# Performance work log

Hardware: AMD Instinct MI355X
Metric: run time of the kernel (lower is better)

Reference implementation:

```python
import jax, jax.numpy as jnp
import numpy as np

H = 512

def _lstm_dir(seq, Wih, Whh, bih, bhh, reverse):
    # seq: [B,S,in]; Wih: [4H,in]; Whh: [4H,H]; biases [4H]
    B = seq.shape[0]
    xp = jnp.einsum('bsi,gi->bsg', seq, Wih) + bih  # precompute input projection [B,S,4H]
    h0 = jnp.zeros((B, H), seq.dtype)
    c0 = jnp.zeros((B, H), seq.dtype)

    def step(carry, xt):
        h, c = carry
        g = xt + h @ Whh.T + bhh
        i, f, gg, o = jnp.split(g, 4, axis=-1)
        c = jax.nn.sigmoid(f) * c + jax.nn.sigmoid(i) * jnp.tanh(gg)
        h = jax.nn.sigmoid(o) * jnp.tanh(c)
        return (h, c), h

    _, hs = jax.lax.scan(step, (h0, c0), jnp.swapaxes(xp, 0, 1), reverse=reverse)
    return jnp.swapaxes(hs, 0, 1)  # [B,S,H]


def setup_inputs() -> dict:
    key = jax.random.key(0)
    ks = jax.random.split(key, 24)
    B, S, E, V, C = 32, 512, 512, 32000, 2
    sc = 0.1
    d = {
        'x': jax.random.randint(ks[0], (B, S), 0, V, dtype=jnp.int32),
        'attention_mask': jnp.ones((B, S), dtype=jnp.int32),
        'emb': jax.random.normal(ks[1], (V, E), jnp.float32) * sc,
        'fc_W': jax.random.normal(ks[2], (C, 2 * H), jnp.float32) * sc,
        'fc_b': jax.random.normal(ks[3], (C,), jnp.float32) * sc,
    }
    i = 4
    for l, insz in [(0, E), (1, 2 * H)]:
        for dname in ('fwd', 'bwd'):
            d[f'{dname}_Wih{l}'] = jax.random.normal(ks[i], (4 * H, insz), jnp.float32) * sc; i += 1
            d[f'{dname}_Whh{l}'] = jax.random.normal(ks[i], (4 * H, H), jnp.float32) * sc; i += 1
            d[f'{dname}_bih{l}'] = jax.random.normal(ks[i], (4 * H,), jnp.float32) * sc; i += 1
            d[f'{dname}_bhh{l}'] = jax.random.normal(ks[i], (4 * H,), jnp.float32) * sc; i += 1
    return d


def reference(x, attention_mask, emb, fc_W, fc_b,
              fwd_Wih0, fwd_Whh0, fwd_bih0, fwd_bhh0,
              bwd_Wih0, bwd_Whh0, bwd_bih0, bwd_bhh0,
              fwd_Wih1, fwd_Whh1, fwd_bih1, fwd_bhh1,
              bwd_Wih1, bwd_Whh1, bwd_bih1, bwd_bhh1):
    out = emb[x]  # [B,S,E]
    layers = [
        ((fwd_Wih0, fwd_Whh0, fwd_bih0, fwd_bhh0), (bwd_Wih0, bwd_Whh0, bwd_bih0, bwd_bhh0)),
        ((fwd_Wih1, fwd_Whh1, fwd_bih1, fwd_bhh1), (bwd_Wih1, bwd_Whh1, bwd_bih1, bwd_bhh1)),
    ]
    for fw, bw in layers:
        f = _lstm_dir(out, *fw, reverse=False)
        b = _lstm_dir(out, *bw, reverse=True)
        out = jnp.concatenate([f, b], axis=-1)  # [B,S,2H]
        # dropout is identity in eval mode
    mask = attention_mask.astype(out.dtype)
    pooled = (out * mask[..., None]).sum(axis=1) / jnp.clip(mask.sum(axis=1, keepdims=True), 1e-9)
    logits = pooled @ fc_W.T + fc_b
    return logits
```

## Files before the change

kernel.cpp:

```cpp
#include <hip/hip_runtime.h>

typedef unsigned short u16;
typedef unsigned int   u32;
typedef unsigned long long u64;
typedef __attribute__((ext_vector_type(8))) short bf16x8;
typedef __attribute__((ext_vector_type(4))) float f32x4;

__device__ __forceinline__ u16 f2bf(float f) {
    u32 u; __builtin_memcpy(&u, &f, 4);
    u32 r = (u + 0x7FFFu + ((u >> 16) & 1u)) >> 16;
    return (u16)r;
}
__device__ __forceinline__ float bf2f(u16 h) {
    u32 u = ((u32)h) << 16; float f; __builtin_memcpy(&f, &u, 4); return f;
}
__device__ __forceinline__ float sigmoidf(float x) { return 1.f / (1.f + __expf(-x)); }
__device__ __forceinline__ float tanh_safe(float x) {
    float e = __expf(-2.f * fabsf(x));
    float t = (1.f - e) / (1.f + e);
    return x >= 0.f ? t : -t;
}

__global__ __launch_bounds__(256) void castk2(const float* __restrict__ s, u16* __restrict__ hi,
                                              u16* __restrict__ lo, int n) {
    int i = blockIdx.x * 256 + threadIdx.x;
    if (i < n) {
        float f = s[i];
        u16 h = f2bf(f);
        hi[i] = h;
        lo[i] = f2bf(f - bf2f(h));
    }
}

__global__ __launch_bounds__(256) void embed_cast(const int* __restrict__ x, const float* __restrict__ emb,
                                                  u16* __restrict__ x0) {
    int m = blockIdx.x;
    int idx = x[m];
    const float2* src = (const float2*)(emb + (size_t)idx * 512);
    u16* dst = x0 + (size_t)m * 512;
    int t = threadIdx.x;
    float2 v = src[t];
    dst[t * 2]     = f2bf(v.x);
    dst[t * 2 + 1] = f2bf(v.y);
}

__global__ __launch_bounds__(256) void gemm_bt(const u16* __restrict__ A, const u16* __restrict__ Bhi,
                                               const u16* __restrict__ Blo,
                                               u16* __restrict__ C, int M, int N, int K) {
    __shared__ __align__(16) u16 sA[128 * 32];
    __shared__ __align__(16) u16 sBh[128 * 32];
    __shared__ __align__(16) u16 sBl[128 * 32];
    const int tid  = threadIdx.x;
    const int lane = tid & 63, wave = tid >> 6;
    const int m0 = blockIdx.y * 128, n0 = blockIdx.x * 128;
    const int wm = (wave >> 1) * 64, wn = (wave & 1) * 64;
    f32x4 acc[4][4] = {};

    const int r0 = tid >> 2, c8 = (tid & 3) * 8;
    const int r1 = r0 + 64;
    const u16* Ap   = A   + (size_t)(m0 + r0) * K + c8;
    const u16* Ap2  = A   + (size_t)(m0 + r1) * K + c8;
    const u16* Bhp  = Bhi + (size_t)(n0 + r0) * K + c8;
    const u16* Bhp2 = Bhi + (size_t)(n0 + r1) * K + c8;
    const u16* Blp  = Blo + (size_t)(n0 + r0) * K + c8;
    const u16* Blp2 = Blo + (size_t)(n0 + r1) * K + c8;

    uint4 ra0, ra1, rh0, rh1, rl0, rl1;
    ra0 = *(const uint4*)(Ap);   ra1 = *(const uint4*)(Ap2);
    rh0 = *(const uint4*)(Bhp);  rh1 = *(const uint4*)(Bhp2);
    rl0 = *(const uint4*)(Blp);  rl1 = *(const uint4*)(Blp2);

    for (int kk = 0; kk < K; kk += 32) {
        __syncthreads();
        *(uint4*)(sA  + tid * 8)        = ra0;
        *(uint4*)(sA  + 2048 + tid * 8) = ra1;
        *(uint4*)(sBh + tid * 8)        = rh0;
        *(uint4*)(sBh + 2048 + tid * 8) = rh1;
        *(uint4*)(sBl + tid * 8)        = rl0;
        *(uint4*)(sBl + 2048 + tid * 8) = rl1;
        int kn = kk + 32;
        if (kn < K) {
            ra0 = *(const uint4*)(Ap + kn);   ra1 = *(const uint4*)(Ap2 + kn);
            rh0 = *(const uint4*)(Bhp + kn);  rh1 = *(const uint4*)(Bhp2 + kn);
            rl0 = *(const uint4*)(Blp + kn);  rl1 = *(const uint4*)(Blp2 + kn);
        }
        __syncthreads();
        bf16x8 av[4], bh[4], bl[4];
#pragma unroll
        for (int i = 0; i < 4; ++i) {
            av[i] = *(const bf16x8*)(sA  + (wm + i * 16 + (lane & 15)) * 32 + (lane >> 4) * 8);
            bh[i] = *(const bf16x8*)(sBh + (wn + i * 16 + (lane & 15)) * 32 + (lane >> 4) * 8);
            bl[i] = *(const bf16x8*)(sBl + (wn + i * 16 + (lane & 15)) * 32 + (lane >> 4) * 8);
        }
#pragma unroll
        for (int i = 0; i < 4; ++i)
#pragma unroll
            for (int j = 0; j < 4; ++j) {
                acc[i][j] = __builtin_amdgcn_mfma_f32_16x16x32_bf16(av[i], bh[j], acc[i][j], 0, 0, 0);
                acc[i][j] = __builtin_amdgcn_mfma_f32_16x16x32_bf16(av[i], bl[j], acc[i][j], 0, 0, 0);
            }
    }
#pragma unroll
    for (int i = 0; i < 4; ++i) {
        int m = m0 + wm + i * 16 + ((lane >> 4) << 2);
#pragma unroll
        for (int j = 0; j < 4; ++j) {
            int n = n0 + wn + j * 16 + (lane & 15);
#pragma unroll
            for (int rr = 0; rr < 4; ++rr)
                C[(size_t)(m + rr) * N + n] = f2bf(acc[i][j][rr]);
        }
    }
}

template <int LAYER>
__global__ __launch_bounds__(256, 1) void lstm_rec(
    const u16* __restrict__ xp_f, const u16* __restrict__ xp_b,
    const u16* __restrict__ whh_f_hi, const u16* __restrict__ whh_f_lo,
    const u16* __restrict__ whh_b_hi, const u16* __restrict__ whh_b_lo,
    const float* __restrict__ bih_f, const float* __restrict__ bhh_f,
    const float* __restrict__ bih_b, const float* __restrict__ bhh_b,
    u16* __restrict__ out0, float* __restrict__ pooled, const int* __restrict__ mask,
    u16* hbuf, u32* cnt)
{
    const int HP = 520;
    __shared__ __align__(16) u16  sHhi[32 * 520];
    __shared__ __align__(16) u16  sHlo[32 * 520];
    __shared__ __align__(16) u16  sXp[32 * 32];
    __shared__ __align__(16) float sG[32 * 33];
    __shared__ __align__(16) u16  sHoutHi[32 * 8];
    __shared__ __align__(16) u16  sHoutLo[32 * 8];

    const int tid = threadIdx.x;
    const int dir = blockIdx.x >> 6;
    const int slice = blockIdx.x & 63;
    const u16* xp     = dir ? xp_b : xp_f;
    const u16* whhH   = dir ? whh_b_hi : whh_f_hi;
    const u16* whhL   = dir ? whh_b_lo : whh_f_lo;
    const float* bih  = dir ? bih_b : bih_f;
    const float* bhh  = dir ? bhh_b : bhh_f;
    u16* hbD = hbuf + dir * 65536;
    u32* myFlags = cnt + dir * 64;

    const int wave = tid >> 6, lane = tid & 63;
    const int wm = (wave >> 1) * 16;
    const int wn = (wave & 1) * 16;
    bf16x8 wfragH[16], wfragL[16];
    {
        int n = wn + (lane & 15);
        int q = n >> 3, rr = n & 7;
        size_t rowoff = (size_t)(q * 512 + slice * 8 + rr) * 512 + (lane >> 4) * 8;
        const u16* wrh = whhH + rowoff;
        const u16* wrl = whhL + rowoff;
#pragma unroll
        for (int k2 = 0; k2 < 16; ++k2) {
            wfragH[k2] = *(const bf16x8*)(wrh + k2 * 32);
            wfragL[k2] = *(const bf16x8*)(wrl + k2 * 32);
        }
    }
    const int b = tid >> 3, r = tid & 7;
    float bias[4];
#pragma unroll
    for (int q = 0; q < 4; ++q) {
        int g = q * 512 + slice * 8 + r;
        bias[q] = bih[g] + bhh[g];
    }
    float cstate = 0.f, pool = 0.f;
    const int aoff = (wm + (lane & 15)) * HP + (lane >> 4) * 8;
    const int gRow = wm + ((lane >> 4) << 2), gCol = wn + (lane & 15);
    const int srow = tid >> 3, sc = tid & 7;

    for (int t = 0; t < 512; ++t) {
        const int tt = dir ? (511 - t) : t;
        if (tid < 128) {
            int xb = tid >> 2, xq = tid & 3;
            const uint4 v = *(const uint4*)(xp + ((size_t)(xb * 512 + tt)) * 2048 + xq * 512 + slice * 8);
            *(uint4*)(sXp + xb * 32 + xq * 8) = v;
        }
        if (t > 0 && tid < 64) {
            const u32 tgt = (u32)t;
            for (;;) {
                u32 v = __hip_atomic_load(myFlags + tid, __ATOMIC_RELAXED, __HIP_MEMORY_SCOPE_AGENT);
                if (__all((int)(v >= tgt))) break;
                __builtin_amdgcn_s_sleep(1);
            }
        }
        __syncthreads();
        if (t > 0) {
            const u16* hp = hbD + ((t - 1) & 1) * 32768 + srow * 512;
            const u16* lp = hp + 16384;
            u16* dhi = sHhi + srow * HP;
            u16* dlo = sHlo + srow * HP;
            u64 rh[16], rl[16];
#pragma unroll
            for (int j = 0; j < 8; ++j) {
                int ch = sc + 8 * j;
                rh[2*j]   = __hip_atomic_load((const u64*)(hp + ch * 8),     __ATOMIC_RELAXED, __HIP_MEMORY_SCOPE_AGENT);
                rh[2*j+1] = __hip_atomic_load((const u64*)(hp + ch * 8) + 1, __ATOMIC_RELAXED, __HIP_MEMORY_SCOPE_AGENT);
                rl[2*j]   = __hip_atomic_load((const u64*)(lp + ch * 8),     __ATOMIC_RELAXED, __HIP_MEMORY_SCOPE_AGENT);
                rl[2*j+1] = __hip_atomic_load((const u64*)(lp + ch * 8) + 1, __ATOMIC_RELAXED, __HIP_MEMORY_SCOPE_AGENT);
            }
#pragma unroll
            for (int j = 0; j < 8; ++j) {
                int ch = sc + 8 * j;
                *(u64*)(dhi + ch * 8)     = rh[2*j];
                *(u64*)(dhi + ch * 8 + 4) = rh[2*j+1];
                *(u64*)(dlo + ch * 8)     = rl[2*j];
                *(u64*)(dlo + ch * 8 + 4) = rl[2*j+1];
            }
        }
        __syncthreads();
        f32x4 acc = {};
        if (t > 0) {
#pragma unroll
            for (int k2 = 0; k2 < 16; ++k2) {
                bf16x8 ah = *(const bf16x8*)(sHhi + aoff + k2 * 32);
                bf16x8 al = *(const bf16x8*)(sHlo + aoff + k2 * 32);
                acc = __builtin_amdgcn_mfma_f32_16x16x32_bf16(ah, wfragH[k2], acc, 0, 0, 0);
                acc = __builtin_amdgcn_mfma_f32_16x16x32_bf16(al, wfragH[k2], acc, 0, 0, 0);
                acc = __builtin_amdgcn_mfma_f32_16x16x32_bf16(ah, wfragL[k2], acc, 0, 0, 0);
            }
        }
#pragma unroll
        for (int rr = 0; rr < 4; ++rr) sG[(gRow + rr) * 33 + gCol] = acc[rr];
        __syncthreads();
        {
            float gq[4];
#pragma unroll
            for (int q = 0; q < 4; ++q)
                gq[q] = sG[b * 33 + q * 8 + r] + bf2f(sXp[b * 32 + q * 8 + r]) + bias[q];
            float ig = sigmoidf(gq[0]), fg = sigmoidf(gq[1]);
            float gg = tanh_safe(gq[2]), og = sigmoidf(gq[3]);
            cstate = fg * cstate + ig * gg;
            float h = og * tanh_safe(cstate);
            u16 hh = f2bf(h);
            if (LAYER == 0) {
                out0[((size_t)(b * 512 + tt)) * 1024 + dir * 512 + slice * 8 + r] = hh;
            } else {
                pool += h * (float)mask[b * 512 + tt];
            }
            sHoutHi[b * 8 + r] = hh;
            sHoutLo[b * 8 + r] = f2bf(h - bf2f(hh));
        }
        __syncthreads();
        if (tid < 64) {
#pragma unroll
            for (int j = 0; j < 2; ++j) {
                int w = tid + 64 * j;
                int pb = w >> 2, d = w & 3;
                u32 vh = ((const u32*)sHoutHi)[w];
                u32 vl = ((const u32*)sHoutLo)[w];
                u32* gh = (u32*)(hbD + (t & 1) * 32768 + pb * 512 + slice * 8) + d;
                u32* gl = (u32*)(hbD + (t & 1) * 32768 + 16384 + pb * 512 + slice * 8) + d;
                __hip_atomic_store(gh, vh, __ATOMIC_RELAXED, __HIP_MEMORY_SCOPE_AGENT);
                __hip_atomic_store(gl, vl, __ATOMIC_RELAXED, __HIP_MEMORY_SCOPE_AGENT);
            }
            if (tid == 0)
                __hip_atomic_store(myFlags + slice, (u32)(t + 1), __ATOMIC_RELEASE, __HIP_MEMORY_SCOPE_AGENT);
        }
    }
    if (LAYER == 1)
        pooled[(size_t)b * 1024 + dir * 512 + slice * 8 + r] = pool;
}

__global__ __launch_bounds__(256) void final_fc(const float* __restrict__ pooled, const int* __restrict__ mask,
                                                const float* __restrict__ fcW, const float* __restrict__ fcb,
                                                float* __restrict__ out) {
    __shared__ float red[256];
    int tid = threadIdx.x;
    int pair = tid & 63, kc = tid >> 6;
    int b = pair >> 1, c = pair & 1;
    float s = 0.f;
    for (int k = kc * 256; k < kc * 256 + 256; ++k)
        s += pooled[b * 1024 + k] * fcW[c * 1024 + k];
    red[tid] = s;
    __syncthreads();
    if (kc == 0) {
        float tot = red[pair] + red[64 + pair] + red[128 + pair] + red[192 + pair];
        float ms = 0.f;
        for (int t = 0; t < 512; ++t) ms += (float)mask[b * 512 + t];
        ms = fmaxf(ms, 1e-9f);
        out[b * 2 + c] = tot / ms + fcb[c];
    }
}

extern "C" void kernel_launch(void* const* d_in, const int* in_sizes, int n_in,
                              void* d_out, int out_size, void* d_ws, size_t ws_size,
                              hipStream_t stream) {
    (void)in_sizes; (void)n_in; (void)out_size; (void)ws_size;
    const int*   x     = (const int*)d_in[0];
    const int*   amask = (const int*)d_in[1];
    const float* emb   = (const float*)d_in[2];
    const float* fcW   = (const float*)d_in[3];
    const float* fcb   = (const float*)d_in[4];
    const float* fWih0 = (const float*)d_in[5];
    const float* fWhh0 = (const float*)d_in[6];
    const float* fbih0 = (const float*)d_in[7];
    const float* fbhh0 = (const float*)d_in[8];
    const float* bWih0 = (const float*)d_in[9];
    const float* bWhh0 = (const float*)d_in[10];
    const float* bbih0 = (const float*)d_in[11];
    const float* bbhh0 = (const float*)d_in[12];
    const float* fWih1 = (const float*)d_in[13];
    const float* fWhh1 = (const float*)d_in[14];
    const float* fbih1 = (const float*)d_in[15];
    const float* fbhh1 = (const float*)d_in[16];
    const float* bWih1 = (const float*)d_in[17];
    const float* bWhh1 = (const float*)d_in[18];
    const float* bbih1 = (const float*)d_in[19];
    const float* bbhh1 = (const float*)d_in[20];

    char* ws = (char*)d_ws;
    size_t off = 0;
    auto alloc = [&](size_t bytes) { void* p = ws + off; off += (bytes + 1023) & ~(size_t)1023; return p; };
    u16* x0    = (u16*)alloc((size_t)16384 * 512 * 2);
    u16* xpf   = (u16*)alloc((size_t)16384 * 2048 * 2);
    u16* xpb   = (u16*)alloc((size_t)16384 * 2048 * 2);
    u16* out0  = (u16*)alloc((size_t)16384 * 1024 * 2);
    u16* wih0fH = (u16*)alloc((size_t)2048 * 512 * 2);
    u16* wih0fL = (u16*)alloc((size_t)2048 * 512 * 2);
    u16* wih0bH = (u16*)alloc((size_t)2048 * 512 * 2);
    u16* wih0bL = (u16*)alloc((size_t)2048 * 512 * 2);
    u16* whh0fH = (u16*)alloc((size_t)2048 * 512 * 2);
    u16* whh0fL = (u16*)alloc((size_t)2048 * 512 * 2);
    u16* whh0bH = (u16*)alloc((size_t)2048 * 512 * 2);
    u16* whh0bL = (u16*)alloc((size_t)2048 * 512 * 2);
    u16* wih1fH = (u16*)alloc((size_t)2048 * 1024 * 2);
    u16* wih1fL = (u16*)alloc((size_t)2048 * 1024 * 2);
    u16* wih1bH = (u16*)alloc((size_t)2048 * 1024 * 2);
    u16* wih1bL = (u16*)alloc((size_t)2048 * 1024 * 2);
    u16* whh1fH = (u16*)alloc((size_t)2048 * 512 * 2);
    u16* whh1fL = (u16*)alloc((size_t)2048 * 512 * 2);
    u16* whh1bH = (u16*)alloc((size_t)2048 * 512 * 2);
    u16* whh1bL = (u16*)alloc((size_t)2048 * 512 * 2);
    float* pooled = (float*)alloc((size_t)32 * 1024 * 4);
    u16* hbuf  = (u16*)alloc((size_t)2 * 2 * 2 * 32 * 512 * 2);
    u32* cnt   = (u32*)alloc(1024);

    hipMemsetAsync(cnt, 0, 1024, stream);

    const int NW0 = 2048 * 512, NW1 = 2048 * 1024;
    castk2<<<dim3((NW0 + 255) / 256), 256, 0, stream>>>(fWih0, wih0fH, wih0fL, NW0);
    castk2<<<dim3((NW0 + 255) / 256), 256, 0, stream>>>(bWih0, wih0bH, wih0bL, NW0);
    castk2<<<dim3((NW0 + 255) / 256), 256, 0, stream>>>(fWhh0, whh0fH, whh0fL, NW0);
    castk2<<<dim3((NW0 + 255) / 256), 256, 0, stream>>>(bWhh0, whh0bH, whh0bL, NW0);
    castk2<<<dim3((NW1 + 255) / 256), 256, 0, stream>>>(fWih1, wih1fH, wih1fL, NW1);
    castk2<<<dim3((NW1 + 255) / 256), 256, 0, stream>>>(bWih1, wih1bH, wih1bL, NW1);
    castk2<<<dim3((NW0 + 255) / 256), 256, 0, stream>>>(fWhh1, whh1fH, whh1fL, NW0);
    castk2<<<dim3((NW0 + 255) / 256), 256, 0, stream>>>(bWhh1, whh1bH, whh1bL, NW0);

    embed_cast<<<dim3(16384), 256, 0, stream>>>(x, emb, x0);

    gemm_bt<<<dim3(16, 128), 256, 0, stream>>>(x0, wih0fH, wih0fL, xpf, 16384, 2048, 512);
    gemm_bt<<<dim3(16, 128), 256, 0, stream>>>(x0, wih0bH, wih0bL, xpb, 16384, 2048, 512);
    lstm_rec<0><<<dim3(128), 256, 0, stream>>>(xpf, xpb, whh0fH, whh0fL, whh0bH, whh0bL,
                                               fbih0, fbhh0, bbih0, bbhh0,
                                               out0, nullptr, nullptr, hbuf, cnt);
    gemm_bt<<<dim3(16, 128), 256, 0, stream>>>(out0, wih1fH, wih1fL, xpf, 16384, 2048, 1024);
    gemm_bt<<<dim3(16, 128), 256, 0, stream>>>(out0, wih1bH, wih1bL, xpb, 16384, 2048, 1024);
    lstm_rec<1><<<dim3(128), 256, 0, stream>>>(xpf, xpb, whh1fH, whh1fL, whh1bH, whh1bL,
                                               fbih1, fbhh1, bbih1, bbhh1,
                                               nullptr, pooled, amask, hbuf, cnt + 128);

    final_fc<<<dim3(1), 256, 0, stream>>>(pooled, amask, fcW, fcb, (float*)d_out);
}
```

Baseline: 7.155 ms.

## Publish hidden state per wave with per-wave flags, drop staging barrier

Each thread now writes its own h hi/lo values straight to the global exchange buffer and each wave raises its own ready flag. This removes the shared-memory staging step and one block-wide barrier from the serial critical path of every timestep. Waiters poll four flags per slice using 64-bit loads. The change also splits the MFMA accumulation into three independent chains to shorten the dependency latency, prefetches xp into registers early, and changes the LDS padding. The flag store is now relaxed rather than release, relying on s_waitcnt for ordering, which carries a memory-ordering risk.

```diff
diff --git a/kernel.cpp b/kernel.cpp
--- a/kernel.cpp
+++ b/kernel.cpp
@@ -123,13 +123,10 @@
     u16* __restrict__ out0, float* __restrict__ pooled, const int* __restrict__ mask,
     u16* hbuf, u32* cnt)
 {
-    const int HP = 520;
-    __shared__ __align__(16) u16  sHhi[32 * 520];
-    __shared__ __align__(16) u16  sHlo[32 * 520];
-    __shared__ __align__(16) u16  sXp[32 * 32];
+    const int HP = 524;
+    __shared__ __align__(16) u16  sHhi[32 * 524];
+    __shared__ __align__(16) u16  sHlo[32 * 524];
     __shared__ __align__(16) float sG[32 * 33];
-    __shared__ __align__(16) u16  sHoutHi[32 * 8];
-    __shared__ __align__(16) u16  sHoutLo[32 * 8];
 
     const int tid = threadIdx.x;
     const int dir = blockIdx.x >> 6;
@@ -140,7 +137,7 @@
     const float* bih  = dir ? bih_b : bih_f;
     const float* bhh  = dir ? bhh_b : bhh_f;
     u16* hbD = hbuf + dir * 65536;
-    u32* myFlags = cnt + dir * 64;
+    u32* myFlags = cnt + dir * 256;
 
     const int wave = tid >> 6, lane = tid & 63;
     const int wm = (wave >> 1) * 16;
@@ -169,19 +166,21 @@
     const int aoff = (wm + (lane & 15)) * HP + (lane >> 4) * 8;
     const int gRow = wm + ((lane >> 4) << 2), gCol = wn + (lane & 15);
     const int srow = tid >> 3, sc = tid & 7;
+    const u16* xpBase = xp + (size_t)(b * 512) * 2048 + slice * 8 + r;
 
     for (int t = 0; t < 512; ++t) {
         const int tt = dir ? (511 - t) : t;
-        if (tid < 128) {
-            int xb = tid >> 2, xq = tid & 3;
-            const uint4 v = *(const uint4*)(xp + ((size_t)(xb * 512 + tt)) * 2048 + xq * 512 + slice * 8);
-            *(uint4*)(sXp + xb * 32 + xq * 8) = v;
-        }
+        const u16* xrow = xpBase + (size_t)tt * 2048;
+        u16 xv0 = xrow[0], xv1 = xrow[512], xv2 = xrow[1024], xv3 = xrow[1536];
         if (t > 0 && tid < 64) {
             const u32 tgt = (u32)t;
+            const u64* fp = (const u64*)(myFlags + tid * 4);
             for (;;) {
-                u32 v = __hip_atomic_load(myFlags + tid, __ATOMIC_RELAXED, __HIP_MEMORY_SCOPE_AGENT);
-                if (__all((int)(v >= tgt))) break;
+                u64 f01 = __hip_atomic_load(fp,     __ATOMIC_RELAXED, __HIP_MEMORY_SCOPE_AGENT);
+                u64 f23 = __hip_atomic_load(fp + 1, __ATOMIC_RELAXED, __HIP_MEMORY_SCOPE_AGENT);
+                int ok = ((u32)f01 >= tgt) & ((u32)(f01 >> 32) >= tgt) &
+                         ((u32)f23 >= tgt) & ((u32)(f23 >> 32) >= tgt);
+                if (__all(ok)) break;
                 __builtin_amdgcn_s_sleep(1);
             }
         }
@@ -210,53 +209,44 @@
             }
         }
         __syncthreads();
-        f32x4 acc = {};
+        f32x4 ac0 = {}, ac1 = {}, ac2 = {};
         if (t > 0) {
 #pragma unroll
             for (int k2 = 0; k2 < 16; ++k2) {
                 bf16x8 ah = *(const bf16x8*)(sHhi + aoff + k2 * 32);
                 bf16x8 al = *(const bf16x8*)(sHlo + aoff + k2 * 32);
-                acc = __builtin_amdgcn_mfma_f32_16x16x32_bf16(ah, wfragH[k2], acc, 0, 0, 0);
-                acc = __builtin_amdgcn_mfma_f32_16x16x32_bf16(al, wfragH[k2], acc, 0, 0, 0);
-                acc = __builtin_amdgcn_mfma_f32_16x16x32_bf16(ah, wfragL[k2], acc, 0, 0, 0);
-            }
-        }
-#pragma unroll
-        for (int rr = 0; rr < 4; ++rr) sG[(gRow + rr) * 33 + gCol] = acc[rr];
+                ac0 = __builtin_amdgcn_mfma_f32_16x16x32_bf16(ah, wfragH[k2], ac0, 0, 0, 0);
+                ac1 = __builtin_amdgcn_mfma_f32_16x16x32_bf16(al, wfragH[k2], ac1, 0, 0, 0);
+                ac2 = __builtin_amdgcn_mfma_f32_16x16x32_bf16(ah, wfragL[k2], ac2, 0, 0, 0);
+            }
+        }
+#pragma unroll
+        for (int rr = 0; rr < 4; ++rr) sG[(gRow + rr) * 33 + gCol] = ac0[rr] + ac1[rr] + ac2[rr];
         __syncthreads();
         {
             float gq[4];
-#pragma unroll
-            for (int q = 0; q < 4; ++q)
-                gq[q] = sG[b * 33 + q * 8 + r] + bf2f(sXp[b * 32 + q * 8 + r]) + bias[q];
+            gq[0] = sG[b * 33 + 0 * 8 + r] + bf2f(xv0) + bias[0];
+            gq[1] = sG[b * 33 + 1 * 8 + r] + bf2f(xv1) + bias[1];
+            gq[2] = sG[b * 33 + 2 * 8 + r] + bf2f(xv2) + bias[2];
+            gq[3] = sG[b * 33 + 3 * 8 + r] + bf2f(xv3) + bias[3];
             float ig = sigmoidf(gq[0]), fg = sigmoidf(gq[1]);
             float gg = tanh_safe(gq[2]), og = sigmoidf(gq[3]);
             cstate = fg * cstate + ig * gg;
             float h = og * tanh_safe(cstate);
             u16 hh = f2bf(h);
+            u16 hl = f2bf(h - bf2f(hh));
             if (LAYER == 0) {
                 out0[((size_t)(b * 512 + tt)) * 1024 + dir * 512 + slice * 8 + r] = hh;
             } else {
                 pool += h * (float)mask[b * 512 + tt];
             }
-            sHoutHi[b * 8 + r] = hh;
-            sHoutLo[b * 8 + r] = f2bf(h - bf2f(hh));
-        }
-        __syncthreads();
-        if (tid < 64) {
-#pragma unroll
-            for (int j = 0; j < 2; ++j) {
-                int w = tid + 64 * j;
-                int pb = w >> 2, d = w & 3;
-                u32 vh = ((const u32*)sHoutHi)[w];
-                u32 vl = ((const u32*)sHoutLo)[w];
-                u32* gh = (u32*)(hbD + (t & 1) * 32768 + pb * 512 + slice * 8) + d;
-                u32* gl = (u32*)(hbD + (t & 1) * 32768 + 16384 + pb * 512 + slice * 8) + d;
-                __hip_atomic_store(gh, vh, __ATOMIC_RELAXED, __HIP_MEMORY_SCOPE_AGENT);
-                __hip_atomic_store(gl, vl, __ATOMIC_RELAXED, __HIP_MEMORY_SCOPE_AGENT);
-            }
-            if (tid == 0)
-                __hip_atomic_store(myFlags + slice, (u32)(t + 1), __ATOMIC_RELEASE, __HIP_MEMORY_SCOPE_AGENT);
+            u16* gh = hbD + (t & 1) * 32768 + b * 512 + slice * 8 + r;
+            __hip_atomic_store(gh,         hh, __ATOMIC_RELAXED, __HIP_MEMORY_SCOPE_AGENT);
+            __hip_atomic_store(gh + 16384, hl, __ATOMIC_RELAXED, __HIP_MEMORY_SCOPE_AGENT);
+            asm volatile("s_waitcnt vmcnt(0)" ::: "memory");
+            if ((tid & 63) == 0)
+                __hip_atomic_store(myFlags + slice * 4 + wave, (u32)(t + 1),
+                                   __ATOMIC_RELAXED, __HIP_MEMORY_SCOPE_AGENT);
         }
     }
     if (LAYER == 1)
@@ -335,9 +325,9 @@
     u16* whh1bL = (u16*)alloc((size_t)2048 * 512 * 2);
     float* pooled = (float*)alloc((size_t)32 * 1024 * 4);
     u16* hbuf  = (u16*)alloc((size_t)2 * 2 * 2 * 32 * 512 * 2);
-    u32* cnt   = (u32*)alloc(1024);
-
-    hipMemsetAsync(cnt, 0, 1024, stream);
+    u32* cnt   = (u32*)alloc(4096);
+
+    hipMemsetAsync(cnt, 0, 4096, stream);
 
     const int NW0 = 2048 * 512, NW1 = 2048 * 1024;
     castk2<<<dim3((NW0 + 255) / 256), 256, 0, stream>>>(fWih0, wih0fH, wih0fL, NW0);
@@ -360,7 +350,7 @@
     gemm_bt<<<dim3(16, 128), 256, 0, stream>>>(out0, wih1bH, wih1bL, xpb, 16384, 2048, 1024);
     lstm_rec<1><<<dim3(128), 256, 0, stream>>>(xpf, xpb, whh1fH, whh1fL, whh1bH, whh1bL,
                                                fbih1, fbhh1, bbih1, bbhh1,
-                                               nullptr, pooled, amask, hbuf, cnt + 128);
+                                               nullptr, pooled, amask, hbuf, cnt + 512);
 
     final_fc<<<dim3(1), 256, 0, stream>>>(pooled, amask, fcW, fcb, (float*)d_out);
 }
```

Result: faster. 6.385 ms (-10.8%).
